# Performance work log

Measured on AMD Instinct MI355X. Metric: run time of the kernel, lower is better.

## Reference

```python
import jax, jax.numpy as jnp
import numpy as np

TWO_PI = 2.0 * np.pi
POW25_7 = 25.0 ** 7
M_RGB2XYZ = np.array([[0.4124564, 0.3575761, 0.1804375],
                      [0.2126729, 0.7151522, 0.072175],
                      [0.0193339, 0.119192, 0.9503041]], dtype=np.float32)
XYZ_REF = np.array([0.95047, 1.0, 1.08883], dtype=np.float32)


def rgb_to_lab(rgb):
    # rgb: [B, 3] in [0, 1]
    lin = jnp.where(rgb > 0.04045, ((rgb + 0.055) / 1.055) ** 2.4, rgb / 12.92)
    xyz = lin @ jnp.asarray(M_RGB2XYZ).T
    xyz_n = xyz / jnp.asarray(XYZ_REF)
    f = jnp.where(xyz_n > 0.008856, jnp.cbrt(xyz_n), 7.787 * xyz_n + 16.0 / 116.0)
    L = 116.0 * f[:, 1] - 16.0
    a = 500.0 * (f[:, 0] - f[:, 1])
    b = 200.0 * (f[:, 1] - f[:, 2])
    return L, a, b


def delta_e_2000(lab1, lab2):
    L1, a1, b1 = lab1
    L2, a2, b2 = lab2
    C1 = jnp.sqrt(a1 ** 2 + b1 ** 2)
    C2 = jnp.sqrt(a2 ** 2 + b2 ** 2)
    C_avg = (C1 + C2) / 2
    C_avg7 = C_avg ** 7
    G = 0.5 * (1 - jnp.sqrt(C_avg7 / (C_avg7 + POW25_7)))
    a1p = a1 * (1 + G)
    a2p = a2 * (1 + G)
    C1p = jnp.sqrt(a1p ** 2 + b1 ** 2)
    C2p = jnp.sqrt(a2p ** 2 + b2 ** 2)
    h1p = jnp.arctan2(b1, a1p) % TWO_PI
    h2p = jnp.arctan2(b2, a2p) % TWO_PI
    dL = L2 - L1
    dC = C2p - C1p
    dh = h2p - h1p
    dh = jnp.where(jnp.abs(dh) > np.pi,
                   jnp.where(h2p <= h1p, dh + TWO_PI, dh - TWO_PI), dh)
    dH = 2 * jnp.sqrt(C1p * C2p) * jnp.sin(dh / 2)
    L_avg = (L1 + L2) / 2
    Cp_avg = (C1p + C2p) / 2
    h_avg = jnp.where(jnp.abs(h1p - h2p) > np.pi,
                      (h1p + h2p + TWO_PI) / 2, (h1p + h2p) / 2)
    T = (1 - 0.17 * jnp.cos(h_avg - np.pi / 6)
         + 0.24 * jnp.cos(2 * h_avg)
         + 0.32 * jnp.cos(3 * h_avg + np.pi / 30)
         - 0.2 * jnp.cos(4 * h_avg - 7 * np.pi / 20))
    theta = 30 * jnp.exp(-(((h_avg * 180.0 / np.pi) - 275.0) / 25.0) ** 2)
    Cp_avg7 = Cp_avg ** 7
    RC = 2 * jnp.sqrt(Cp_avg7 / (Cp_avg7 + POW25_7))
    RT = -jnp.sin(2 * theta) * RC
    SL = 1 + 0.015 * (L_avg - 50) ** 2 / jnp.sqrt(20 + (L_avg - 50) ** 2)
    SC = 1 + 0.045 * Cp_avg
    SH = 1 + 0.015 * Cp_avg * T
    return jnp.sqrt((dL / SL) ** 2 + (dC / SC) ** 2 + (dH / SH) ** 2
                    + RT * (dC / SC) * (dH / SH))


def setup_inputs() -> dict:
    key = jax.random.key(0)
    k1, k2 = jax.random.split(key)
    B = 16777216
    pred = jax.random.uniform(k1, (B, 3), dtype=jnp.float32)
    target = jax.random.uniform(k2, (B, 3), dtype=jnp.float32)
    return {"pred": pred, "target": target}


def reference(pred, target):
    mse_loss = jnp.mean((pred - target) ** 2, axis=1)  # [B]
    de = delta_e_2000(rgb_to_lab(pred), rgb_to_lab(target))  # [B]
    # original detaches delta_e (computed on CPU numpy, written into a new tensor)
    combined = 0.2 * mse_loss + 0.8 * jax.lax.stop_gradient(de)
    return jnp.mean(combined)
```

## Files before the change

kernel.cpp:

```cpp
#include <hip/hip_runtime.h>
#include <math.h>

#define TPB 256
#define MAXBLOCKS 8192

typedef float v4f __attribute__((ext_vector_type(4)));

__device__ __forceinline__ float fsqrt_(float x){ return __builtin_amdgcn_sqrtf(x); }
__device__ __forceinline__ float frcp_ (float x){ return __builtin_amdgcn_rcpf(x); }
__device__ __forceinline__ float frsq_ (float x){ return __builtin_amdgcn_rsqf(x); }
__device__ __forceinline__ float flog2_(float x){ return __builtin_amdgcn_logf(x); }
__device__ __forceinline__ float fexp2_(float x){ return __builtin_amdgcn_exp2f(x); }
__device__ __forceinline__ float fsinr_(float x){ return __builtin_amdgcn_sinf(x); }

__device__ __forceinline__ v4f vs(float x){ return (v4f){x, x, x, x}; }

#define V4APPLY(fn, a) ((v4f){ fn((a).x), fn((a).y), fn((a).z), fn((a).w) })
__device__ __forceinline__ v4f vsqrt(v4f a){ return V4APPLY(fsqrt_, a); }
__device__ __forceinline__ v4f vrcp (v4f a){ return V4APPLY(frcp_ , a); }
__device__ __forceinline__ v4f vrsq (v4f a){ return V4APPLY(frsq_ , a); }
__device__ __forceinline__ v4f vlog2(v4f a){ return V4APPLY(flog2_, a); }
__device__ __forceinline__ v4f vexp2(v4f a){ return V4APPLY(fexp2_, a); }
__device__ __forceinline__ v4f vsinr(v4f a){ return V4APPLY(fsinr_, a); }

#if __has_builtin(__builtin_elementwise_fma)
__device__ __forceinline__ v4f vfma(v4f a, v4f b, v4f c){ return __builtin_elementwise_fma(a,b,c); }
#else
__device__ __forceinline__ v4f vfma(v4f a, v4f b, v4f c){ return a*b + c; }
#endif
__device__ __forceinline__ v4f vmax(v4f a, v4f b){ return __builtin_elementwise_max(a,b); }
__device__ __forceinline__ v4f vmin(v4f a, v4f b){ return __builtin_elementwise_min(a,b); }
__device__ __forceinline__ v4f vabs(v4f a){ return __builtin_elementwise_abs(a); }
__device__ __forceinline__ v4f vselgt(v4f x, float t, v4f a, v4f b){
    v4f r;
    r.x = x.x > t ? a.x : b.x;
    r.y = x.y > t ? a.y : b.y;
    r.z = x.z > t ? a.z : b.z;
    r.w = x.w > t ? a.w : b.w;
    return r;
}
__device__ __forceinline__ v4f vcopysign(v4f m, v4f s){
    v4f r;
    r.x = copysignf(m.x, s.x);
    r.y = copysignf(m.y, s.y);
    r.z = copysignf(m.z, s.z);
    r.w = copysignf(m.w, s.w);
    return r;
}

__device__ __forceinline__ v4f srgb_lin(v4f c){
    v4f t = (c + vs(0.055f)) * vs(1.0f/1.055f);
    v4f p = vexp2(vs(2.4f) * vlog2(t));
    return vselgt(c, 0.04045f, p, c * vs(1.0f/12.92f));
}
__device__ __forceinline__ v4f lab_f(v4f t){
    v4f cb = vexp2(vs(1.0f/3.0f) * vlog2(t));
    return vselgt(t, 0.008856f, cb, vfma(vs(7.787f), t, vs(16.0f/116.0f)));
}

__device__ __forceinline__ void rgb2lab(v4f r, v4f g, v4f b, v4f& L, v4f& A, v4f& Bv){
    v4f lr = srgb_lin(r), lg = srgb_lin(g), lb = srgb_lin(b);
    v4f xn = vfma(vs(0.4339499f), lr, vfma(vs(0.3762098f), lg, vs(0.1898414f)*lb));
    v4f yn = vfma(vs(0.2126729f), lr, vfma(vs(0.7151522f), lg, vs(0.0721750f)*lb));
    v4f zn = vfma(vs(0.0177566f), lr, vfma(vs(0.1094680f), lg, vs(0.8727720f)*lb));
    v4f fx = lab_f(xn), fy = lab_f(yn), fz = lab_f(zn);
    L  = vfma(vs(116.0f), fy, vs(-16.0f));
    A  = vs(500.0f) * (fx - fy);
    Bv = vs(200.0f) * (fy - fz);
}

__device__ __forceinline__ v4f vatan2_2pi(v4f y, v4f x){
    v4f ax = vabs(x), ay = vabs(y);
    v4f mx = vmax(ax, ay), mn = vmin(ax, ay);
    v4f t = mn * vrcp(vmax(mx, vs(1e-38f)));
    v4f s = t * t;
    v4f p = vs(-0.01172120f);
    p = vfma(p, s, vs( 0.05265332f));
    p = vfma(p, s, vs(-0.11643287f));
    p = vfma(p, s, vs( 0.19354346f));
    p = vfma(p, s, vs(-0.33262347f));
    p = vfma(p, s, vs( 0.99997726f));
    p = p * t;
    v4f r = vselgt(ay - ax, 0.0f, vs(1.57079632679f) - p, p);
    r = vselgt(vs(0.0f) - x, 0.0f, vs(3.14159265359f) - r, r);
    r = vselgt(vs(0.0f) - y, 0.0f, vs(6.28318530718f) - r, r);
    return r;
}

__device__ __forceinline__ v4f row_loss(v4f pr, v4f pg, v4f pb,
                                        v4f tr, v4f tg, v4f tb){
    const float P257 = 6103515625.0f;

    v4f dr = pr - tr, dg = pg - tg, db = pb - tb;
    v4f mse = (dr*dr + dg*dg + db*db) * vs(1.0f/3.0f);

    v4f L1, a1, b1, L2, a2, b2;
    rgb2lab(pr, pg, pb, L1, a1, b1);
    rgb2lab(tr, tg, tb, L2, a2, b2);

    v4f C1 = vsqrt(vfma(a1, a1, b1*b1));
    v4f C2 = vsqrt(vfma(a2, a2, b2*b2));
    v4f Cav = vs(0.5f) * (C1 + C2);
    v4f c2v = Cav*Cav;
    v4f c7 = c2v*c2v*c2v*Cav;
    v4f gs = vsqrt(c7 * vrcp(c7 + vs(P257)));
    v4f opG = vfma(vs(-0.5f), gs, vs(1.5f));
    v4f a1p = a1 * opG;
    v4f a2p = a2 * opG;
    v4f C1p = vsqrt(vfma(a1p, a1p, b1*b1));
    v4f C2p = vsqrt(vfma(a2p, a2p, b2*b2));

    v4f dL = L2 - L1;
    v4f dC = C2p - C1p;

    v4f prod  = C1p * C2p;
    v4f dot   = vfma(a1p, a2p, b1*b2);
    v4f cross = vfma(a1p, b2, vs(0.0f) - a2p*b1);
    v4f dH = vcopysign(vsqrt(vmax(vs(2.0f)*(prod - dot), vs(0.0f))), cross);

    v4f Lav  = vs(0.5f) * (L1 + L2);
    v4f Cpav = vs(0.5f) * (C1p + C2p);

    v4f vx = vfma(a1p, C2p, a2p*C1p);
    v4f vy = vfma(b1 , C2p, b2 *C1p);
    v4f hav = vatan2_2pi(vy, vx);
    v4f inv = vrsq(vmax(vfma(vx, vx, vy*vy), vs(1e-30f)));
    v4f ch = vx * inv, sh = vy * inv;

    v4f cos2 = vfma(vs(2.0f)*ch, ch, vs(-1.0f));
    v4f sin2 = vs(2.0f) * sh * ch;
    v4f cos3 = ch * vfma(vs(2.0f), cos2, vs(-1.0f));
    v4f sin3 = sh * vfma(vs(2.0f), cos2, vs( 1.0f));
    v4f cos4 = vfma(vs(2.0f)*cos2, cos2, vs(-1.0f));
    v4f sin4 = vs(2.0f) * sin2 * cos2;
    v4f T = vs(1.0f);
    T = vfma(vs(-0.147224319f), ch,   T);
    T = vfma(vs(-0.085f),       sh,   T);
    T = vfma(vs( 0.24f),        cos2, T);
    T = vfma(vs( 0.318247006f), cos3, T);
    T = vfma(vs(-0.033449109f), sin3, T);
    T = vfma(vs(-0.090798100f), cos4, T);
    T = vfma(vs(-0.178201305f), sin4, T);

    v4f u = vfma(hav, vs(2.29183118f), vs(-11.0f));
    v4f theta = vs(30.0f) * vexp2(vs(-1.44269504f) * (u*u));

    v4f cp2 = Cpav*Cpav;
    v4f cp7 = cp2*cp2*cp2*Cpav;
    v4f RC = vs(2.0f) * vsqrt(cp7 * vrcp(cp7 + vs(P257)));
    v4f RT = vs(0.0f) - vsinr(theta * vs(0.31830988618f)) * RC;

    v4f Lm = Lav - vs(50.0f);
    v4f Lm2 = Lm * Lm;
    v4f SL = vfma(vs(0.015f) * Lm2, vrsq(vs(20.0f) + Lm2), vs(1.0f));
    v4f SC = vfma(vs(0.045f), Cpav, vs(1.0f));
    v4f SH = vfma(vs(0.015f) * Cpav, T, vs(1.0f));

    v4f t1 = dL * vrcp(SL);
    v4f t2 = dC * vrcp(SC);
    v4f t3 = dH * vrcp(SH);
    v4f arg = vfma(t1, t1, vfma(t2, t2, vfma(t3, t3, RT*t2*t3)));
    v4f de = vsqrt(vmax(arg, vs(0.0f)));

    return vfma(vs(0.2f), mse, vs(0.8f) * de);
}

__global__ void __launch_bounds__(TPB)
de_main(const float* __restrict__ pred, const float* __restrict__ tgt,
        float* __restrict__ partials, int B){
    int nvec = B >> 2;
    int gid = blockIdx.x * TPB + threadIdx.x;
    int stride = gridDim.x * TPB;
    v4f acc4 = vs(0.0f);

    for (int i = gid; i < nvec; i += stride){
        const float4* p4 = (const float4*)pred + (size_t)i * 3;
        const float4* t4 = (const float4*)tgt  + (size_t)i * 3;
        float4 pA = p4[0], pB = p4[1], pC = p4[2];
        float4 tA = t4[0], tB = t4[1], tC = t4[2];
        v4f pr = (v4f){pA.x, pA.w, pB.z, pC.y};
        v4f pg = (v4f){pA.y, pB.x, pB.w, pC.z};
        v4f pb = (v4f){pA.z, pB.y, pC.x, pC.w};
        v4f qr = (v4f){tA.x, tA.w, tB.z, tC.y};
        v4f qg = (v4f){tA.y, tB.x, tB.w, tC.z};
        v4f qb = (v4f){tA.z, tB.y, tC.x, tC.w};
        acc4 += row_loss(pr, pg, pb, qr, qg, qb);
    }
    float acc = acc4.x + acc4.y + acc4.z + acc4.w;

    int r = (nvec << 2) + gid;
    if (r < B){
        v4f pr = vs(pred[(size_t)r*3]), pg = vs(pred[(size_t)r*3+1]), pb = vs(pred[(size_t)r*3+2]);
        v4f qr = vs(tgt [(size_t)r*3]), qg = vs(tgt [(size_t)r*3+1]), qb = vs(tgt [(size_t)r*3+2]);
        acc += row_loss(pr, pg, pb, qr, qg, qb).x;
    }

    __shared__ float sdata[TPB];
    sdata[threadIdx.x] = acc;
    __syncthreads();
    #pragma unroll
    for (int s = TPB/2; s > 0; s >>= 1){
        if (threadIdx.x < s) sdata[threadIdx.x] += sdata[threadIdx.x + s];
        __syncthreads();
    }
    if (threadIdx.x == 0) partials[blockIdx.x] = sdata[0];
}

__global__ void __launch_bounds__(TPB)
de_final(const float* __restrict__ partials, int n, float* __restrict__ out, double invB){
    __shared__ double sd[TPB];
    double acc = 0.0;
    for (int i = threadIdx.x; i < n; i += TPB) acc += (double)partials[i];
    sd[threadIdx.x] = acc;
    __syncthreads();
    #pragma unroll
    for (int s = TPB/2; s > 0; s >>= 1){
        if (threadIdx.x < s) sd[threadIdx.x] += sd[threadIdx.x + s];
        __syncthreads();
    }
    if (threadIdx.x == 0) out[0] = (float)(sd[0] * invB);
}

extern "C" void kernel_launch(void* const* d_in, const int* in_sizes, int n_in,
                              void* d_out, int out_size, void* d_ws, size_t ws_size,
                              hipStream_t stream){
    const float* pred = (const float*)d_in[0];
    const float* tgt  = (const float*)d_in[1];
    int B = in_sizes[0] / 3;

    int nvec = B >> 2;
    int blocks = (nvec + TPB - 1) / TPB;
    if (blocks > MAXBLOCKS) blocks = MAXBLOCKS;
    size_t wcap = ws_size / sizeof(float);
    if (wcap > 0 && (size_t)blocks > wcap) blocks = (int)wcap;
    if (blocks < 1) blocks = 1;

    float* partials = (float*)d_ws;
    de_main <<<blocks, TPB, 0, stream>>>(pred, tgt, partials, B);
    de_final<<<1, TPB, 0, stream>>>(partials, blocks, (float*)d_out, 1.0/(double)B);
}
```

Measured before the change: 417.1 us.

## Software-prefetch next quad, cut transcendentals, shrink grid to fewer blocks

The grid-stride loop now loads the next iteration's six float4s before computing the current one. This is meant to overlap global-memory latency with the heavy per-row math. The sqrt(x/(x+c)) terms are rewritten as x*rsqrt(x*(x+c)), and the three reciprocals of SL/SC/SH are merged into one reciprocal plus multiplies, to cut special-function instructions. The grid cap drops from 8192 to 2048 blocks so each thread does more iterations. The prefetch raises register pressure and may lower occupancy, and the smaller grid reduces latency hiding across waves.

After: 421.7 us. Within noise of the previous version (+1.1%).

```diff
diff --git a/kernel.cpp b/kernel.cpp
--- a/kernel.cpp
+++ b/kernel.cpp
@@ -2,7 +2,7 @@
 #include <math.h>
 
 #define TPB 256
-#define MAXBLOCKS 8192
+#define NBLOCKS 2048
 
 typedef float v4f __attribute__((ext_vector_type(4)));
 
@@ -103,7 +103,7 @@
     v4f Cav = vs(0.5f) * (C1 + C2);
     v4f c2v = Cav*Cav;
     v4f c7 = c2v*c2v*c2v*Cav;
-    v4f gs = vsqrt(c7 * vrcp(c7 + vs(P257)));
+    v4f gs = c7 * vrsq(vmax(c7*(c7 + vs(P257)), vs(1e-30f)));
     v4f opG = vfma(vs(-0.5f), gs, vs(1.5f));
     v4f a1p = a1 * opG;
     v4f a2p = a2 * opG;
@@ -147,7 +147,7 @@
 
     v4f cp2 = Cpav*Cpav;
     v4f cp7 = cp2*cp2*cp2*Cpav;
-    v4f RC = vs(2.0f) * vsqrt(cp7 * vrcp(cp7 + vs(P257)));
+    v4f RC = vs(2.0f) * (cp7 * vrsq(vmax(cp7*(cp7 + vs(P257)), vs(1e-30f))));
     v4f RT = vs(0.0f) - vsinr(theta * vs(0.31830988618f)) * RC;
 
     v4f Lm = Lav - vs(50.0f);
@@ -156,13 +156,39 @@
     v4f SC = vfma(vs(0.045f), Cpav, vs(1.0f));
     v4f SH = vfma(vs(0.015f) * Cpav, T, vs(1.0f));
 
-    v4f t1 = dL * vrcp(SL);
-    v4f t2 = dC * vrcp(SC);
-    v4f t3 = dH * vrcp(SH);
+    v4f SCSH = SC * SH;
+    v4f SLSH = SL * SH;
+    v4f SLSC = SL * SC;
+    v4f R = vrcp(SLSC * SH);
+    v4f t1 = dL * (SCSH * R);
+    v4f t2 = dC * (SLSH * R);
+    v4f t3 = dH * (SLSC * R);
     v4f arg = vfma(t1, t1, vfma(t2, t2, vfma(t3, t3, RT*t2*t3)));
     v4f de = vsqrt(vmax(arg, vs(0.0f)));
 
     return vfma(vs(0.2f), mse, vs(0.8f) * de);
+}
+
+struct Quad { float4 a, b, c, d, e, f; };
+
+__device__ __forceinline__ Quad load_quad(const float* __restrict__ pred,
+                                          const float* __restrict__ tgt, int i){
+    const float4* p4 = (const float4*)pred + (size_t)i * 3;
+    const float4* t4 = (const float4*)tgt  + (size_t)i * 3;
+    Quad q;
+    q.a = p4[0]; q.b = p4[1]; q.c = p4[2];
+    q.d = t4[0]; q.e = t4[1]; q.f = t4[2];
+    return q;
+}
+
+__device__ __forceinline__ v4f quad_loss(const Quad& q){
+    v4f pr = (v4f){q.a.x, q.a.w, q.b.z, q.c.y};
+    v4f pg = (v4f){q.a.y, q.b.x, q.b.w, q.c.z};
+    v4f pb = (v4f){q.a.z, q.b.y, q.c.x, q.c.w};
+    v4f qr = (v4f){q.d.x, q.d.w, q.e.z, q.f.y};
+    v4f qg = (v4f){q.d.y, q.e.x, q.e.w, q.f.z};
+    v4f qb = (v4f){q.d.z, q.e.y, q.f.x, q.f.w};
+    return row_loss(pr, pg, pb, qr, qg, qb);
 }
 
 __global__ void __launch_bounds__(TPB)
@@ -173,18 +199,18 @@
     int stride = gridDim.x * TPB;
     v4f acc4 = vs(0.0f);
 
-    for (int i = gid; i < nvec; i += stride){
-        const float4* p4 = (const float4*)pred + (size_t)i * 3;
-        const float4* t4 = (const float4*)tgt  + (size_t)i * 3;
-        float4 pA = p4[0], pB = p4[1], pC = p4[2];
-        float4 tA = t4[0], tB = t4[1], tC = t4[2];
-        v4f pr = (v4f){pA.x, pA.w, pB.z, pC.y};
-        v4f pg = (v4f){pA.y, pB.x, pB.w, pC.z};
-        v4f pb = (v4f){pA.z, pB.y, pC.x, pC.w};
-        v4f qr = (v4f){tA.x, tA.w, tB.z, tC.y};
-        v4f qg = (v4f){tA.y, tB.x, tB.w, tC.z};
-        v4f qb = (v4f){tA.z, tB.y, tC.x, tC.w};
-        acc4 += row_loss(pr, pg, pb, qr, qg, qb);
+    int i = gid;
+    bool valid = (i < nvec);
+    Quad cur;
+    if (valid) cur = load_quad(pred, tgt, i);
+    #pragma unroll 1
+    while (valid){
+        int j = i + stride;
+        bool jv = (j < nvec);
+        Quad nxt;
+        if (jv) nxt = load_quad(pred, tgt, j);
+        acc4 += quad_loss(cur);
+        cur = nxt; i = j; valid = jv;
     }
     float acc = acc4.x + acc4.y + acc4.z + acc4.w;
 
@@ -230,7 +256,7 @@
 
     int nvec = B >> 2;
     int blocks = (nvec + TPB - 1) / TPB;
-    if (blocks > MAXBLOCKS) blocks = MAXBLOCKS;
+    if (blocks > NBLOCKS) blocks = NBLOCKS;
     size_t wcap = ws_size / sizeof(float);
     if (wcap > 0 && (size_t)blocks > wcap) blocks = (int)wcap;
     if (blocks < 1) blocks = 1;
```
